# Kernel optimization log

Measured on AMD Instinct MI355X. Metric: run time of the kernel, lower is better.

The kernel has to match this reference:

```python
import jax, jax.numpy as jnp
import numpy as np
import math

D_MODEL = 2048
N_HEADS = 16
D_HEAD = D_MODEL // N_HEADS
SCALE = 1.0 / math.sqrt(D_HEAD)


def setup_inputs() -> dict:
    key = jax.random.key(0)
    kx, kq, kk, kv, ko = jax.random.split(key, 5)
    x = jax.random.normal(kx, (2, 2048, D_MODEL), dtype=jnp.float32)
    W_q = jax.random.normal(kq, (D_MODEL, D_MODEL), dtype=jnp.float32)
    W_k = jax.random.normal(kk, (D_MODEL, D_MODEL), dtype=jnp.float32)
    W_v = jax.random.normal(kv, (D_MODEL, D_MODEL), dtype=jnp.float32) * math.sqrt(2.0 / D_MODEL)
    W_o = jax.random.normal(ko, (D_MODEL, D_MODEL), dtype=jnp.float32) * math.sqrt(2.0 / D_MODEL)
    return {"x": x, "W_q": W_q, "W_k": W_k, "W_v": W_v, "W_o": W_o}


def reference(x, W_q, W_k, W_v, W_o) -> jnp.ndarray:
    B, S, D = x.shape
    q = (x @ W_q).reshape(B, S, N_HEADS, D_HEAD)  # [b, q, h, dh]
    k = (x @ W_k).reshape(B, S, N_HEADS, D_HEAD)  # [b, k, h, dh]
    v = x @ W_v                                    # [b, k, d_model] (NOT split into heads)
    scores = jnp.einsum('bqhd,bkhd->bhqk', q, k)   # [b, h, q, k]
    # Faithful quirk: additive -1e9 causal mask applied BEFORE the scale.
    mask = jnp.triu(jnp.full((S, S), -1e9, dtype=scores.dtype), k=1)
    scores = (scores + mask) * SCALE
    probs = jax.nn.softmax(scores, axis=-1)
    # Faithful quirk: sums over heads h AND keys k against full-width v.
    out = jnp.einsum('bhqk,bkd->bqd', probs, v)    # [b, q, d_model]
    return out @ W_o
```

## Files before the change

### kernel.cpp

```cpp
#include <hip/hip_runtime.h>

typedef unsigned short u16;
typedef __attribute__((ext_vector_type(8))) short bf16x8;
typedef __attribute__((ext_vector_type(4))) float f32x4;

#define DEV __device__ __forceinline__
#define EXP2(x) __builtin_amdgcn_exp2f(x)
#define LOG2(x) __builtin_amdgcn_logf(x)

DEV u16 f2bf(float f) {
  union { float f; unsigned u; } v; v.f = f;
  unsigned r = v.u + 0x7fffu + ((v.u >> 16) & 1u);
  return (u16)(r >> 16);
}
DEV float bf2f(u16 h) {
  union { unsigned u; float f; } v; v.u = ((unsigned)h) << 16;
  return v.f;
}
DEV f32x4 mfma16(bf16x8 a, bf16x8 b, f32x4 c) {
  return __builtin_amdgcn_mfma_f32_16x16x32_bf16(a, b, c, 0, 0, 0);
}
DEV void cp16(const u16* g, u16* l) {
  __builtin_amdgcn_global_load_lds((__attribute__((address_space(1))) void*)g,
                                   (__attribute__((address_space(3))) void*)l, 16, 0, 0);
}

__global__ __launch_bounds__(256) void split_pair(const float4* __restrict__ x,
                                                  u16* __restrict__ hi, u16* __restrict__ lo) {
  const size_t i = (size_t)blockIdx.x * 256 + threadIdx.x;
  const float4 v = x[i];
  ushort4 h, l;
  h.x = f2bf(v.x); l.x = f2bf(v.x - bf2f(h.x));
  h.y = f2bf(v.y); l.y = f2bf(v.y - bf2f(h.y));
  h.z = f2bf(v.z); l.z = f2bf(v.z - bf2f(h.z));
  h.w = f2bf(v.w); l.w = f2bf(v.w - bf2f(h.w));
  *(ushort4*)&hi[i * 4] = h;
  *(ushort4*)&lo[i * 4] = l;
}

template<bool LO>
__global__ __launch_bounds__(256) void transpose_split(const float* __restrict__ W,
                                                       u16* __restrict__ Th, u16* __restrict__ Tl) {
  __shared__ float t[64][65];
  const int r0 = blockIdx.y * 64, c0 = blockIdx.x * 64;
  const int rr = threadIdx.x >> 4, c4 = (threadIdx.x & 15) * 4;
#pragma unroll
  for (int p = 0; p < 4; ++p) {
    const float4 v = *(const float4*)&W[(size_t)(r0 + p * 16 + rr) * 2048 + c0 + c4];
    t[p * 16 + rr][c4 + 0] = v.x; t[p * 16 + rr][c4 + 1] = v.y;
    t[p * 16 + rr][c4 + 2] = v.z; t[p * 16 + rr][c4 + 3] = v.w;
  }
  __syncthreads();
#pragma unroll
  for (int p = 0; p < 4; ++p) {
    const int cc = p * 16 + rr;
    const float v0 = t[c4 + 0][cc], v1 = t[c4 + 1][cc], v2 = t[c4 + 2][cc], v3 = t[c4 + 3][cc];
    ushort4 h;
    h.x = f2bf(v0); h.y = f2bf(v1); h.z = f2bf(v2); h.w = f2bf(v3);
    *(ushort4*)&Th[(size_t)(c0 + cc) * 2048 + r0 + c4] = h;
    if constexpr (LO) {
      ushort4 l;
      l.x = f2bf(v0 - bf2f(h.x)); l.y = f2bf(v1 - bf2f(h.y));
      l.z = f2bf(v2 - bf2f(h.z)); l.w = f2bf(v3 - bf2f(h.w));
      *(ushort4*)&Tl[(size_t)(c0 + cc) * 2048 + r0 + c4] = l;
    }
  }
}

template<bool SPLIT3, int OUTMODE, bool KLIM>
__global__ __launch_bounds__(256, 2) void gemm_bt(
    const u16* __restrict__ Aph, const u16* __restrict__ Apl,
    const u16* __restrict__ Bph, const u16* __restrict__ Bpl,
    void* __restrict__ C0, void* __restrict__ C1,
    const int M, const int N, const int K, const int bShift) {
  extern __shared__ u16 lds[];
  constexpr int T_AL = 4096;
  constexpr int T_BH = SPLIT3 ? 8192 : 4096;
  constexpr int T_BL = 12288;
  const int tid = threadIdx.x;
  const int wave = tid >> 6, lane = tid & 63;
  const int li = lane & 15, l4 = lane >> 4;
  const int m0 = blockIdx.y * 128, n0 = blockIdx.x * 128;
  const int wr = (wave >> 1) * 64, wc = (wave & 1) * 64;
  const u16* Bh = Bph; const u16* Bl = Bpl;
  if (bShift) { const size_t s = (size_t)(m0 >> 11) * (size_t)bShift; Bh += s; if (SPLIT3) Bl += s; }

  const f32x4 fz = {0.f, 0.f, 0.f, 0.f};
  f32x4 acc[4][4];
#pragma unroll
  for (int m = 0; m < 4; ++m)
#pragma unroll
    for (int n = 0; n < 4; ++n) acc[m][n] = fz;

  const size_t aoff = (size_t)(m0 + (tid >> 2)) * K + (tid & 3) * 8;
  const size_t boff = (size_t)(n0 + (tid >> 2)) * K + (tid & 3) * 8;
  const size_t rstep = (size_t)64 * K;
  const int s0 = tid * 8, s1 = 2048 + tid * 8;
  const int abase = (wr + li) * 32 + l4 * 8;
  const int bbase = (wc + li) * 32 + l4 * 8;
  const int kEnd = KLIM ? ((m0 & 2047) + 128 < K ? (m0 & 2047) + 128 : K) : K;

#pragma unroll 1
  for (int k0 = 0; k0 < kEnd; k0 += 32) {
    cp16(Aph + aoff + k0,         &lds[s0]);
    cp16(Aph + aoff + rstep + k0, &lds[s1]);
    cp16(Bh + boff + k0,          &lds[T_BH + s0]);
    cp16(Bh + boff + rstep + k0,  &lds[T_BH + s1]);
    if constexpr (SPLIT3) {
      cp16(Apl + aoff + k0,         &lds[T_AL + s0]);
      cp16(Apl + aoff + rstep + k0, &lds[T_AL + s1]);
      cp16(Bl + boff + k0,          &lds[T_BL + s0]);
      cp16(Bl + boff + rstep + k0,  &lds[T_BL + s1]);
    }
    __syncthreads();
    bf16x8 af[4], bf_[4];
#pragma unroll
    for (int m = 0; m < 4; ++m) af[m] = *(const bf16x8*)&lds[abase + m * 512];
#pragma unroll
    for (int n = 0; n < 4; ++n) bf_[n] = *(const bf16x8*)&lds[T_BH + bbase + n * 512];
    if constexpr (SPLIT3) {
      bf16x8 alf[4], blf[4];
#pragma unroll
      for (int m = 0; m < 4; ++m) alf[m] = *(const bf16x8*)&lds[T_AL + abase + m * 512];
#pragma unroll
      for (int n = 0; n < 4; ++n) blf[n] = *(const bf16x8*)&lds[T_BL + bbase + n * 512];
#pragma unroll
      for (int m = 0; m < 4; ++m)
#pragma unroll
        for (int n = 0; n < 4; ++n) {
          acc[m][n] = mfma16(af[m], bf_[n], acc[m][n]);
          acc[m][n] = mfma16(af[m], blf[n], acc[m][n]);
          acc[m][n] = mfma16(alf[m], bf_[n], acc[m][n]);
        }
    } else {
#pragma unroll
      for (int m = 0; m < 4; ++m)
#pragma unroll
        for (int n = 0; n < 4; ++n)
          acc[m][n] = mfma16(af[m], bf_[n], acc[m][n]);
    }
    __syncthreads();
  }

#pragma unroll
  for (int m = 0; m < 4; ++m) {
#pragma unroll
    for (int n = 0; n < 4; ++n) {
      const int rg0 = m0 + wr + m * 16 + l4 * 4;
      const int cg  = n0 + wc + n * 16 + li;
      if constexpr (OUTMODE == 0) {
        u16* Ch = (u16*)C0; u16* Cl = (u16*)C1;
#pragma unroll
        for (int r = 0; r < 4; ++r) {
          const float v = acc[m][n][r];
          const u16 h = f2bf(v);
          Ch[(size_t)(rg0 + r) * N + cg] = h;
          Cl[(size_t)(rg0 + r) * N + cg] = f2bf(v - bf2f(h));
        }
      } else if constexpr (OUTMODE == 1) {
        u16* Cs = (u16*)C0;
#pragma unroll
        for (int r = 0; r < 4; ++r) Cs[(size_t)(rg0 + r) * N + cg] = f2bf(acc[m][n][r]);
      } else if constexpr (OUTMODE == 2) {
        u16* Vt = (u16*)C0;
        ushort4 pk;
        pk.x = f2bf(acc[m][n][0]); pk.y = f2bf(acc[m][n][1]);
        pk.z = f2bf(acc[m][n][2]); pk.w = f2bf(acc[m][n][3]);
        *(ushort4*)&Vt[(size_t)(rg0 >> 11) * 4194304 + (size_t)cg * 2048 + (rg0 & 2047)] = pk;
      } else {
        float* Cf = (float*)C0;
#pragma unroll
        for (int r = 0; r < 4; ++r) Cf[(size_t)(rg0 + r) * N + cg] = acc[m][n][r];
      }
    }
  }
}

#define C2EXP 0.1275174381027786f

__global__ __launch_bounds__(256) void attn_lse_part(
    const u16* __restrict__ Qh, const u16* __restrict__ Ql,
    const u16* __restrict__ Kh, const u16* __restrict__ Kl,
    float* __restrict__ Mp, float* __restrict__ Lp) {
  const int j = blockIdx.x, qt = 15 - (int)blockIdx.y, hb = blockIdx.z;
  const int b = hb >> 4, h = hb & 15;
  const int tid = threadIdx.x;
  const int nch = (qt >> 2) + 1;
  if (j >= nch) {
    if (tid < 128) {
      const size_t o = ((size_t)hb * 4 + j) * 2048 + qt * 128 + tid;
      Mp[o] = -3.0e38f; Lp[o] = 0.f;
    }
    return;
  }
  __shared__ __align__(16) u16 kb[16384];
  const int wave = tid >> 6, lane = tid & 63;
  const int li = lane & 15, l4 = lane >> 4;
  const int q0w = qt * 128 + wave * 32;
  const int rs = ((li << 6) | (l4 << 4)) ^ (((li >> 1) & 7) << 4);

  bf16x8 qfh[2][4], qfl[2][4];
#pragma unroll
  for (int mf = 0; mf < 2; ++mf) {
    const size_t qo = ((size_t)(b * 2048 + q0w + mf * 16 + li)) * 2048 + h * 128 + l4 * 8;
#pragma unroll
    for (int ks = 0; ks < 4; ++ks) {
      qfh[mf][ks] = *(const bf16x8*)&Qh[qo + ks * 32];
      qfl[mf][ks] = *(const bf16x8*)&Ql[qo + ks * 32];
    }
  }
  float m[2][4], l[2][4];
#pragma unroll
  for (int mf = 0; mf < 2; ++mf)
#pragma unroll
    for (int r = 0; r < 4; ++r) { m[mf][r] = -3.0e38f; l[mf][r] = 0.f; }

  const int kst = j * 8;
  const int ken = min(j * 8 + 8, qt * 2 + 2);
  const size_t kgbase = ((size_t)b * 2048) * 2048 + h * 128;
  const f32x4 fz = {0.f, 0.f, 0.f, 0.f};

#pragma unroll 1
  for (int t = kst; t < ken; ++t) {
    __syncthreads();
#pragma unroll
    for (int i = 0; i < 4; ++i) {
      const int o = (tid + i * 256) * 16;
      const int op = o ^ (((o >> 7) & 7) << 4);
      const int dck = op >> 12, s = (op >> 6) & 63, dl = (op >> 1) & 31;
      const size_t g = kgbase + (size_t)(t * 64 + s) * 2048 + dck * 32 + dl;
      cp16(Kh + g, kb + (o >> 1));
      cp16(Kl + g, kb + 8192 + (o >> 1));
    }
    __syncthreads();
#pragma unroll
    for (int sn = 0; sn < 4; ++sn) {
      f32x4 a0 = fz, a1 = fz;
#pragma unroll
      for (int ks = 0; ks < 4; ++ks) {
        const bf16x8 kh = *(const bf16x8*)((const char*)kb + ks * 4096 + (sn << 10) + rs);
        const bf16x8 kl = *(const bf16x8*)((const char*)kb + 16384 + ks * 4096 + (sn << 10) + rs);
        a0 = mfma16(qfh[0][ks], kh, a0);
        a0 = mfma16(qfh[0][ks], kl, a0);
        a0 = mfma16(qfl[0][ks], kh, a0);
        a1 = mfma16(qfh[1][ks], kh, a1);
        a1 = mfma16(qfh[1][ks], kl, a1);
        a1 = mfma16(qfl[1][ks], kh, a1);
      }
      const int kg = t * 64 + sn * 16 + li;
#pragma unroll
      for (int r = 0; r < 4; ++r) {
        if (kg <= q0w + l4 * 4 + r) {
          const float mn = fmaxf(m[0][r], a0[r]);
          l[0][r] = l[0][r] * EXP2((m[0][r] - mn) * C2EXP) + EXP2((a0[r] - mn) * C2EXP);
          m[0][r] = mn;
        }
        if (kg <= q0w + 16 + l4 * 4 + r) {
          const float mn = fmaxf(m[1][r], a1[r]);
          l[1][r] = l[1][r] * EXP2((m[1][r] - mn) * C2EXP) + EXP2((a1[r] - mn) * C2EXP);
          m[1][r] = mn;
        }
      }
    }
  }
#pragma unroll
  for (int off = 1; off <= 8; off <<= 1) {
#pragma unroll
    for (int mf = 0; mf < 2; ++mf)
#pragma unroll
      for (int r = 0; r < 4; ++r) {
        const float om = __shfl_xor(m[mf][r], off, 64);
        const float ol = __shfl_xor(l[mf][r], off, 64);
        const float mn = fmaxf(m[mf][r], om);
        l[mf][r] = l[mf][r] * EXP2((m[mf][r] - mn) * C2EXP) + ol * EXP2((om - mn) * C2EXP);
        m[mf][r] = mn;
      }
  }
  if (li == 0) {
#pragma unroll
    for (int mf = 0; mf < 2; ++mf)
#pragma unroll
      for (int r = 0; r < 4; ++r) {
        const size_t o = ((size_t)hb * 4 + j) * 2048 + q0w + mf * 16 + l4 * 4 + r;
        Mp[o] = m[mf][r];
        Lp[o] = l[mf][r];
      }
  }
}

__global__ __launch_bounds__(256) void attn_lse_merge(
    const float* __restrict__ Mp, const float* __restrict__ Lp, float* __restrict__ LSE) {
  const int id = blockIdx.x * 256 + threadIdx.x;
  const int q = id & 2047, hb = id >> 11;
  const size_t base = (size_t)hb * 4 * 2048 + q;
  float m = Mp[base], l = Lp[base];
#pragma unroll
  for (int jj = 1; jj < 4; ++jj) {
    const float om = Mp[base + jj * 2048];
    const float ol = Lp[base + jj * 2048];
    const float mn = fmaxf(m, om);
    l = l * EXP2((m - mn) * C2EXP) + ol * EXP2((om - mn) * C2EXP);
    m = mn;
  }
  LSE[(size_t)hb * 2048 + q] = m * C2EXP + LOG2(l);
}

__global__ __launch_bounds__(256) void attn_psum(
    const u16* __restrict__ Qh, const u16* __restrict__ Ql,
    const u16* __restrict__ Kh, const u16* __restrict__ Kl,
    const float* __restrict__ LSE, u16* __restrict__ Psum) {
  const int kt = blockIdx.x, qt = blockIdx.y, b = blockIdx.z;
  const int q0 = qt * 128, k0 = kt * 128;
  const int tid = threadIdx.x;

  if (kt > qt) {
    const size_t o = ((size_t)(b * 2048 + q0 + (tid >> 1))) * 2048 + k0 + (tid & 1) * 64;
    const uint4 z = {0u, 0u, 0u, 0u};
#pragma unroll
    for (int j = 0; j < 8; ++j) *(uint4*)&Psum[o + j * 8] = z;
    return;
  }

  extern __shared__ u16 kb2[];
  const int wave = tid >> 6, lane = tid & 63;
  const int li = lane & 15, l4 = lane >> 4;
  const int q0w = q0 + wave * 32;
  const int rs = ((li << 6) | (l4 << 4)) ^ (((li >> 1) & 7) << 4);
  const int snmax = (kt == qt) ? (wave * 2 + 2) : 8;

  const f32x4 fz = {0.f, 0.f, 0.f, 0.f};
  f32x4 ps[2][8];
#pragma unroll
  for (int mf = 0; mf < 2; ++mf)
#pragma unroll
    for (int sn = 0; sn < 8; ++sn) ps[mf][sn] = fz;

  const size_t kgbase = ((size_t)(b * 2048 + k0)) * 2048;
  const size_t qbase0 = ((size_t)(b * 2048 + q0w + li)) * 2048 + l4 * 8;
  const size_t qbase1 = qbase0 + (size_t)16 * 2048;
  const size_t lbase  = (size_t)(b * 16) * 2048 + q0w + l4 * 4;

#pragma unroll 1
  for (int h = 0; h < 16; ++h) {
    __syncthreads();
#pragma unroll
    for (int i = 0; i < 8; ++i) {
      const int o = (tid + i * 256) * 16;
      const int op = o ^ (((o >> 7) & 7) << 4);
      const int dck = op >> 13, s = (op >> 6) & 127, dl = (op >> 1) & 31;
      const size_t g = kgbase + (size_t)s * 2048 + h * 128 + dck * 32 + dl;
      cp16(Kh + g, kb2 + (o >> 1));
      cp16(Kl + g, kb2 + 16384 + (o >> 1));
    }
    bf16x8 qfh0[4], qfl0[4], qfh1[4], qfl1[4];
    float clse[2][4];
#pragma unroll
    for (int ks = 0; ks < 4; ++ks) {
      qfh0[ks] = *(const bf16x8*)&Qh[qbase0 + (size_t)h * 128 + ks * 32];
      qfl0[ks] = *(const bf16x8*)&Ql[qbase0 + (size_t)h * 128 + ks * 32];
      qfh1[ks] = *(const bf16x8*)&Qh[qbase1 + (size_t)h * 128 + ks * 32];
      qfl1[ks] = *(const bf16x8*)&Ql[qbase1 + (size_t)h * 128 + ks * 32];
    }
#pragma unroll
    for (int mf = 0; mf < 2; ++mf)
#pragma unroll
      for (int r = 0; r < 4; ++r)
        clse[mf][r] = LSE[lbase + (size_t)h * 2048 + mf * 16 + r];
    __syncthreads();

#pragma unroll
    for (int sn = 0; sn < 8; ++sn) {
      if (sn < snmax) {
        f32x4 a0 = fz, a1 = fz;
#pragma unroll
        for (int ks = 0; ks < 4; ++ks) {
          const bf16x8 kh = *(const bf16x8*)((const char*)kb2 + ks * 8192 + (sn << 10) + rs);
          const bf16x8 kl = *(const bf16x8*)((const char*)kb2 + 32768 + ks * 8192 + (sn << 10) + rs);
          a0 = mfma16(qfh0[ks], kh, a0);
          a0 = mfma16(qfh0[ks], kl, a0);
          a0 = mfma16(qfl0[ks], kh, a0);
          a1 = mfma16(qfh1[ks], kh, a1);
          a1 = mfma16(qfh1[ks], kl, a1);
          a1 = mfma16(qfl1[ks], kh, a1);
        }
        const int kg = k0 + sn * 16 + li;
#pragma unroll
        for (int r = 0; r < 4; ++r) {
          if (kg <= q0w + l4 * 4 + r)      ps[0][sn][r] += EXP2(a0[r] * C2EXP - clse[0][r]);
          if (kg <= q0w + 16 + l4 * 4 + r) ps[1][sn][r] += EXP2(a1[r] * C2EXP - clse[1][r]);
        }
      }
    }
  }

#pragma unroll
  for (int mf = 0; mf < 2; ++mf)
#pragma unroll
    for (int sn = 0; sn < 8; ++sn) {
      const size_t o0 = ((size_t)(b * 2048 + q0w + mf * 16 + l4 * 4)) * 2048 + k0 + sn * 16 + li;
#pragma unroll
      for (int r = 0; r < 4; ++r) Psum[o0 + (size_t)r * 2048] = f2bf(ps[mf][sn][r]);
    }
}

extern "C" void kernel_launch(void* const* d_in, const int* in_sizes, int n_in,
                              void* d_out, int out_size, void* d_ws, size_t ws_size,
                              hipStream_t stream) {
  (void)in_sizes; (void)n_in; (void)out_size; (void)ws_size;
  const float* x  = (const float*)d_in[0];
  const float* Wq = (const float*)d_in[1];
  const float* Wk = (const float*)d_in[2];
  const float* Wv = (const float*)d_in[3];
  const float* Wo = (const float*)d_in[4];
  u16* ws = (u16*)d_ws;
  const size_t E8 = 8388608, E4 = 4194304;
  u16* xh = ws;
  u16* xl = ws + E8;
  u16* Qh = ws + 2 * E8;
  u16* Ql = ws + 3 * E8;
  u16* Kh = ws + 4 * E8;
  u16* Kl = ws + 5 * E8;
  u16* Vt = ws + 6 * E8;
  u16* WTh = ws + 7 * E8;
  u16* WTl = ws + 7 * E8 + E4;
  u16* WTb = ws + 7 * E8 + 2 * E4;
  float* LSEf = (float*)WTl;
  float* Mp   = LSEf + 65536;
  float* Lp   = Mp + 262144;
  u16* Psum = xl;
  u16* out1 = xh;

  split_pair<<<8192, 256, 0, stream>>>((const float4*)x, xh, xl);

  dim3 tg(32, 32);
  dim3 gg(16, 32);

  transpose_split<true ><<<tg, 256, 0, stream>>>(Wq, WTh, WTl);
  gemm_bt<true, 0, false><<<gg, 256, 32768, stream>>>(xh, xl, WTh, WTl, Qh, Ql, 4096, 2048, 2048, 0);

  transpose_split<true ><<<tg, 256, 0, stream>>>(Wk, WTh, WTl);
  gemm_bt<true, 0, false><<<gg, 256, 32768, stream>>>(xh, xl, WTh, WTl, Kh, Kl, 4096, 2048, 2048, 0);

  transpose_split<false><<<tg, 256, 0, stream>>>(Wv, WTb, nullptr);
  gemm_bt<false, 2, false><<<gg, 256, 16384, stream>>>(xh, nullptr, WTb, nullptr, Vt, nullptr, 4096, 2048, 2048, 0);

  attn_lse_part<<<dim3(4, 16, 32), 256, 0, stream>>>(Qh, Ql, Kh, Kl, Mp, Lp);
  attn_lse_merge<<<256, 256, 0, stream>>>(Mp, Lp, LSEf);
  attn_psum<<<dim3(16, 16, 2), 256, 65536, stream>>>(Qh, Ql, Kh, Kl, LSEf, Psum);

  gemm_bt<false, 1, true><<<gg, 256, 16384, stream>>>(Psum, nullptr, Vt, nullptr, out1, nullptr, 4096, 2048, 2048, 4194304);

  transpose_split<false><<<tg, 256, 0, stream>>>(Wo, WTb, nullptr);
  gemm_bt<false, 3, false><<<gg, 256, 16384, stream>>>(out1, nullptr, WTb, nullptr, d_out, nullptr, 4096, 2048, 2048, 0);
}
```

Measured before the change: 602.1 us.

## Batch Q/K projections in one launch, remap GEMM tiles per XCD, skip masked LSE tiles

Q and K projection GEMMs now run as one launch with blockIdx.z choosing the weight and output buffers. The Wk transpose is staged into the V buffer so all three transposes run first. GEMM blocks are remapped so each of the 8 XCDs gets a contiguous set of M tiles, for better L2 reuse of A rows. The LSE partial kernel skips 16-key subtiles that lie fully above the causal diagonal, and takes a cheap wave-uniform path when no lane's running max changes, avoiding rescale exponentials.

```diff
diff --git a/kernel.cpp b/kernel.cpp
--- a/kernel.cpp
+++ b/kernel.cpp
@@ -71,16 +71,22 @@
 __global__ __launch_bounds__(256, 2) void gemm_bt(
     const u16* __restrict__ Aph, const u16* __restrict__ Apl,
     const u16* __restrict__ Bph, const u16* __restrict__ Bpl,
+    const u16* __restrict__ Bph2, const u16* __restrict__ Bpl2,
     void* __restrict__ C0, void* __restrict__ C1,
+    void* __restrict__ C0b, void* __restrict__ C1b,
     const int M, const int N, const int K, const int bShift) {
   extern __shared__ u16 lds[];
   constexpr int T_AL = 4096;
   constexpr int T_BH = SPLIT3 ? 8192 : 4096;
   constexpr int T_BL = 12288;
+  if (blockIdx.z) { Bph = Bph2; Bpl = Bpl2; C0 = C0b; C1 = C1b; }
   const int tid = threadIdx.x;
   const int wave = tid >> 6, lane = tid & 63;
   const int li = lane & 15, l4 = lane >> 4;
-  const int m0 = blockIdx.y * 128, n0 = blockIdx.x * 128;
+  const int lin0 = ((int)blockIdx.y << 4) | (int)blockIdx.x;
+  const int xcd = lin0 & 7, idx = lin0 >> 3;
+  const int m0 = ((xcd << 2) | (idx & 3)) * 128;
+  const int n0 = (idx >> 2) * 128;
   const int wr = (wave >> 1) * 64, wc = (wave & 1) * 64;
   const u16* Bh = Bph; const u16* Bl = Bpl;
   if (bShift) { const size_t s = (size_t)(m0 >> 11) * (size_t)bShift; Bh += s; if (SPLIT3) Bl += s; }
@@ -235,30 +241,42 @@
     __syncthreads();
 #pragma unroll
     for (int sn = 0; sn < 4; ++sn) {
-      f32x4 a0 = fz, a1 = fz;
-#pragma unroll
-      for (int ks = 0; ks < 4; ++ks) {
-        const bf16x8 kh = *(const bf16x8*)((const char*)kb + ks * 4096 + (sn << 10) + rs);
-        const bf16x8 kl = *(const bf16x8*)((const char*)kb + 16384 + ks * 4096 + (sn << 10) + rs);
-        a0 = mfma16(qfh[0][ks], kh, a0);
-        a0 = mfma16(qfh[0][ks], kl, a0);
-        a0 = mfma16(qfl[0][ks], kh, a0);
-        a1 = mfma16(qfh[1][ks], kh, a1);
-        a1 = mfma16(qfh[1][ks], kl, a1);
-        a1 = mfma16(qfl[1][ks], kh, a1);
-      }
-      const int kg = t * 64 + sn * 16 + li;
-#pragma unroll
-      for (int r = 0; r < 4; ++r) {
-        if (kg <= q0w + l4 * 4 + r) {
-          const float mn = fmaxf(m[0][r], a0[r]);
-          l[0][r] = l[0][r] * EXP2((m[0][r] - mn) * C2EXP) + EXP2((a0[r] - mn) * C2EXP);
-          m[0][r] = mn;
-        }
-        if (kg <= q0w + 16 + l4 * 4 + r) {
-          const float mn = fmaxf(m[1][r], a1[r]);
-          l[1][r] = l[1][r] * EXP2((m[1][r] - mn) * C2EXP) + EXP2((a1[r] - mn) * C2EXP);
-          m[1][r] = mn;
+      if (64 * t + 16 * sn <= q0w + 31) {
+        f32x4 a0 = fz, a1 = fz;
+#pragma unroll
+        for (int ks = 0; ks < 4; ++ks) {
+          const bf16x8 kh = *(const bf16x8*)((const char*)kb + ks * 4096 + (sn << 10) + rs);
+          const bf16x8 kl = *(const bf16x8*)((const char*)kb + 16384 + ks * 4096 + (sn << 10) + rs);
+          a0 = mfma16(qfh[0][ks], kh, a0);
+          a0 = mfma16(qfh[0][ks], kl, a0);
+          a0 = mfma16(qfl[0][ks], kh, a0);
+          a1 = mfma16(qfh[1][ks], kh, a1);
+          a1 = mfma16(qfh[1][ks], kl, a1);
+          a1 = mfma16(qfl[1][ks], kh, a1);
+        }
+        const int kg = t * 64 + sn * 16 + li;
+#pragma unroll
+        for (int r = 0; r < 4; ++r) {
+          {
+            const float aa = (kg <= q0w + l4 * 4 + r) ? a0[r] : -3.3e38f;
+            if (__all(aa <= m[0][r])) {
+              l[0][r] += EXP2((aa - m[0][r]) * C2EXP);
+            } else {
+              const float mn = fmaxf(m[0][r], aa);
+              l[0][r] = l[0][r] * EXP2((m[0][r] - mn) * C2EXP) + EXP2((aa - mn) * C2EXP);
+              m[0][r] = mn;
+            }
+          }
+          {
+            const float aa = (kg <= q0w + 16 + l4 * 4 + r) ? a1[r] : -3.3e38f;
+            if (__all(aa <= m[1][r])) {
+              l[1][r] += EXP2((aa - m[1][r]) * C2EXP);
+            } else {
+              const float mn = fmaxf(m[1][r], aa);
+              l[1][r] = l[1][r] * EXP2((m[1][r] - mn) * C2EXP) + EXP2((aa - mn) * C2EXP);
+              m[1][r] = mn;
+            }
+          }
         }
       }
     }
@@ -317,7 +335,7 @@
     const size_t o = ((size_t)(b * 2048 + q0 + (tid >> 1))) * 2048 + k0 + (tid & 1) * 64;
     const uint4 z = {0u, 0u, 0u, 0u};
 #pragma unroll
-    for (int j = 0; j < 8; ++j) *(uint4*)&Psum[o + j * 8] = z;
+    for (int j2 = 0; j2 < 8; ++j2) *(uint4*)&Psum[o + j2 * 8] = z;
     return;
   }
 
@@ -424,6 +442,8 @@
   u16* WTh = ws + 7 * E8;
   u16* WTl = ws + 7 * E8 + E4;
   u16* WTb = ws + 7 * E8 + 2 * E4;
+  u16* WkTh = Vt;
+  u16* WkTl = Vt + E4;
   float* LSEf = (float*)WTl;
   float* Mp   = LSEf + 65536;
   float* Lp   = Mp + 262144;
@@ -433,23 +453,28 @@
   split_pair<<<8192, 256, 0, stream>>>((const float4*)x, xh, xl);
 
   dim3 tg(32, 32);
-  dim3 gg(16, 32);
 
   transpose_split<true ><<<tg, 256, 0, stream>>>(Wq, WTh, WTl);
-  gemm_bt<true, 0, false><<<gg, 256, 32768, stream>>>(xh, xl, WTh, WTl, Qh, Ql, 4096, 2048, 2048, 0);
-
-  transpose_split<true ><<<tg, 256, 0, stream>>>(Wk, WTh, WTl);
-  gemm_bt<true, 0, false><<<gg, 256, 32768, stream>>>(xh, xl, WTh, WTl, Kh, Kl, 4096, 2048, 2048, 0);
-
+  transpose_split<true ><<<tg, 256, 0, stream>>>(Wk, WkTh, WkTl);
   transpose_split<false><<<tg, 256, 0, stream>>>(Wv, WTb, nullptr);
-  gemm_bt<false, 2, false><<<gg, 256, 16384, stream>>>(xh, nullptr, WTb, nullptr, Vt, nullptr, 4096, 2048, 2048, 0);
+
+  gemm_bt<true, 0, false><<<dim3(16, 32, 2), 256, 32768, stream>>>(
+      xh, xl, WTh, WTl, WkTh, WkTl, Qh, Ql, Kh, Kl, 4096, 2048, 2048, 0);
+
+  gemm_bt<false, 2, false><<<dim3(16, 32), 256, 16384, stream>>>(
+      xh, nullptr, WTb, nullptr, nullptr, nullptr, Vt, nullptr, nullptr, nullptr,
+      4096, 2048, 2048, 0);
 
   attn_lse_part<<<dim3(4, 16, 32), 256, 0, stream>>>(Qh, Ql, Kh, Kl, Mp, Lp);
   attn_lse_merge<<<256, 256, 0, stream>>>(Mp, Lp, LSEf);
   attn_psum<<<dim3(16, 16, 2), 256, 65536, stream>>>(Qh, Ql, Kh, Kl, LSEf, Psum);
 
-  gemm_bt<false, 1, true><<<gg, 256, 16384, stream>>>(Psum, nullptr, Vt, nullptr, out1, nullptr, 4096, 2048, 2048, 4194304);
+  gemm_bt<false, 1, true><<<dim3(16, 32), 256, 16384, stream>>>(
+      Psum, nullptr, Vt, nullptr, nullptr, nullptr, out1, nullptr, nullptr, nullptr,
+      4096, 2048, 2048, 4194304);
 
   transpose_split<false><<<tg, 256, 0, stream>>>(Wo, WTb, nullptr);
-  gemm_bt<false, 3, false><<<gg, 256, 16384, stream>>>(out1, nullptr, WTb, nullptr, d_out, nullptr, 4096, 2048, 2048, 0);
-}
+  gemm_bt<false, 3, false><<<dim3(16, 32), 256, 16384, stream>>>(
+      out1, nullptr, WTb, nullptr, nullptr, nullptr, d_out, nullptr, nullptr, nullptr,
+      4096, 2048, 2048, 0);
+}
```

Result: slower. 616.3 us (+2.4%).
